# Kernel tuning notes

Hardware: AMD Instinct MI355X
Metric: run time of the kernel (lower is better)

## Reference

```python
import jax, jax.numpy as jnp
import numpy as np

N_NODES = 100000
N_EDGES = 1600000


def setup_inputs() -> dict:
    key = jax.random.key(0)
    k1, k2, k3, k4 = jax.random.split(key, 4)
    x = jax.random.normal(k1, (N_NODES, 128), dtype=jnp.float32)
    edge_idx = jax.random.randint(k2, (2, N_EDGES), 0, N_NODES, dtype=jnp.int64)
    W1 = jax.random.normal(k3, (128, 64), dtype=jnp.float32) * (1.0 / np.sqrt(128))
    b1 = jnp.zeros((64,), dtype=jnp.float32)
    W2 = jax.random.normal(k4, (64, 40), dtype=jnp.float32) * (1.0 / np.sqrt(64))
    b2 = jnp.zeros((40,), dtype=jnp.float32)
    return {"x": x, "edge_idx": edge_idx, "W1": W1, "b1": b1, "W2": W2, "b2": b2}


def _gcn_conv(x, src, dst, norm, W, b, n_nodes):
    # x @ W -> gather by src, scale by symmetric norm, scatter-add to dst, + bias
    h = x @ W                               # [N, d_out]
    msg = h[src] * norm[:, None]            # [E+N, d_out]
    out = jax.ops.segment_sum(msg, dst, num_segments=n_nodes)
    return out + b


def _norm_and_loops(edge_idx, n_nodes):
    # PyG GCNConv default: add self-loops, norm = deg^-1/2[src] * deg^-1/2[dst]
    loops = jnp.arange(n_nodes, dtype=edge_idx.dtype)
    src = jnp.concatenate([edge_idx[0], loops])
    dst = jnp.concatenate([edge_idx[1], loops])
    deg = jnp.zeros((n_nodes,), jnp.float32).at[dst].add(1.0)
    dinv = jnp.where(deg > 0, jax.lax.rsqrt(deg), 0.0)
    norm = dinv[src] * dinv[dst]
    return src, dst, norm


def reference(x, edge_idx, W1, b1, W2, b2):
    n_nodes = x.shape[0]
    src, dst, norm = _norm_and_loops(edge_idx, n_nodes)
    hidden = jax.nn.relu(_gcn_conv(x, src, dst, norm, W1, b1, n_nodes))
    # dropout is a no-op in eval mode (training=False)
    return _gcn_conv(hidden, src, dst, norm, W2, b2, n_nodes)
```

## Files before the change

kernel.cpp:

```cpp
#include <hip/hip_runtime.h>

#define D_IN  128
#define D_HID 64
#define D_OUT 40

__global__ __launch_bounds__(256) void k_deg(const int* __restrict__ dst,
                                             unsigned int* __restrict__ cnt,
                                             unsigned int* __restrict__ rank, int E) {
    int e = blockIdx.x * 256 + threadIdx.x;
    if (e < E) rank[e] = atomicAdd(&cnt[dst[e]], 1u);
}

__global__ __launch_bounds__(256) void k_dinv(const unsigned int* __restrict__ deg,
                                              float* __restrict__ dinv, int N) {
    int i = blockIdx.x * 256 + threadIdx.x;
    if (i < N) dinv[i] = rsqrtf((float)(deg[i] + 1u));
}

__global__ __launch_bounds__(256) void k_scan1(const unsigned int* __restrict__ deg,
                                               unsigned int* __restrict__ off,
                                               unsigned int* __restrict__ bsum, int N) {
    __shared__ unsigned int s[256];
    const int tid = threadIdx.x;
    const int i = blockIdx.x * 256 + tid;
    unsigned int v = (i < N) ? deg[i] : 0u;
    s[tid] = v;
    __syncthreads();
    for (int d = 1; d < 256; d <<= 1) {
        unsigned int t = (tid >= d) ? s[tid - d] : 0u;
        __syncthreads();
        s[tid] += t;
        __syncthreads();
    }
    if (i < N) off[i] = s[tid] - v;
    if (tid == 255) bsum[blockIdx.x] = s[tid];
}

__global__ __launch_bounds__(512) void k_scan2(unsigned int* __restrict__ bsum, int NB) {
    __shared__ unsigned int s[512];
    const int tid = threadIdx.x;
    unsigned int v = (tid < NB) ? bsum[tid] : 0u;
    s[tid] = v;
    __syncthreads();
    for (int d = 1; d < 512; d <<= 1) {
        unsigned int t = (tid >= d) ? s[tid - d] : 0u;
        __syncthreads();
        s[tid] += t;
        __syncthreads();
    }
    if (tid < NB) bsum[tid] = s[tid] - v;
}

__global__ __launch_bounds__(256) void k_scan3(unsigned int* __restrict__ off,
                                               const unsigned int* __restrict__ bsum,
                                               int N, int E) {
    int i = blockIdx.x * 256 + threadIdx.x;
    if (i < N) off[i] += bsum[blockIdx.x];
    if (i == 0) off[N] = (unsigned int)E;
}

__global__ __launch_bounds__(256) void k_fill(const int* __restrict__ src,
                                              const int* __restrict__ dst,
                                              const unsigned int* __restrict__ off,
                                              const unsigned int* __restrict__ rank,
                                              int* __restrict__ csr_src, int E) {
    int e = blockIdx.x * 256 + threadIdx.x;
    if (e >= E) return;
    csr_src[off[dst[e]] + rank[e]] = src[e];
}

__global__ __launch_bounds__(256) void k_gemm1(const float* __restrict__ x,
                                               const float* __restrict__ W1,
                                               const float* __restrict__ dinv,
                                               float* __restrict__ h1s, int N) {
    __shared__ float w[D_IN * D_HID];
    __shared__ float xs[16][D_IN + 4];
    const int tid = threadIdx.x;
    const float4* W4 = (const float4*)W1;
    float4* w4 = (float4*)w;
    for (int i = tid; i < D_IN * D_HID / 4; i += 256) w4[i] = W4[i];
    const int row0 = blockIdx.x * 16;
    const float4* X4 = (const float4*)(x + (size_t)row0 * D_IN);
    for (int i = tid; i < 16 * D_IN / 4; i += 256) {
        float4 v = X4[i];
        int r = i >> 5;
        int k = (i & 31) * 4;
        *(float4*)&xs[r][k] = v;
    }
    __syncthreads();
    const int r  = tid >> 4;
    const int c4 = (tid & 15) * 4;
    float a0 = 0, a1 = 0, a2 = 0, a3 = 0;
#pragma unroll 8
    for (int k = 0; k < D_IN; ++k) {
        float  xv = xs[r][k];
        float4 wv = *(const float4*)&w[k * D_HID + c4];
        a0 = fmaf(xv, wv.x, a0);
        a1 = fmaf(xv, wv.y, a1);
        a2 = fmaf(xv, wv.z, a2);
        a3 = fmaf(xv, wv.w, a3);
    }
    const int row = row0 + r;
    if (row < N) {
        float dv = dinv[row];
        float4 o = {a0 * dv, a1 * dv, a2 * dv, a3 * dv};
        *(float4*)&h1s[(size_t)row * D_HID + c4] = o;
    }
}

__global__ __launch_bounds__(320) void k_gemm2(const float* __restrict__ hid,
                                               const float* __restrict__ W2,
                                               const float* __restrict__ dinv,
                                               float* __restrict__ h2s, int N) {
    __shared__ float w[D_HID * D_OUT];
    __shared__ float xs[16][D_HID + 4];
    const int tid = threadIdx.x;
    const float2* W22 = (const float2*)W2;
    float2* w2 = (float2*)w;
    for (int i = tid; i < D_HID * D_OUT / 2; i += 320) w2[i] = W22[i];
    const int row0 = blockIdx.x * 16;
    const float4* X4 = (const float4*)(hid + (size_t)row0 * D_HID);
    for (int i = tid; i < 16 * D_HID / 4; i += 320) {
        float4 v = X4[i];
        int r = i >> 4;
        int k = (i & 15) * 4;
        *(float4*)&xs[r][k] = v;
    }
    __syncthreads();
    const int r  = tid / 20;
    const int c2 = (tid % 20) * 2;
    float a0 = 0, a1 = 0;
#pragma unroll 8
    for (int k = 0; k < D_HID; ++k) {
        float  xv = xs[r][k];
        float2 wv = *(const float2*)&w[k * D_OUT + c2];
        a0 = fmaf(xv, wv.x, a0);
        a1 = fmaf(xv, wv.y, a1);
    }
    const int row = row0 + r;
    if (row < N) {
        float dv = dinv[row];
        float2 o = {a0 * dv, a1 * dv};
        *(float2*)&h2s[(size_t)row * D_OUT + c2] = o;
    }
}

__global__ __launch_bounds__(256) void k_gather1(const unsigned int* __restrict__ off,
                                                 const int* __restrict__ csr_src,
                                                 const float* __restrict__ h1s,
                                                 const float* __restrict__ dinv,
                                                 const float* __restrict__ b1,
                                                 float* __restrict__ hidden, int N) {
    const int wid  = (blockIdx.x * 256 + threadIdx.x) >> 6;
    const int lane = threadIdx.x & 63;
    if (wid >= N) return;
    const int start = (int)off[wid];
    const int end   = (int)off[wid + 1];
    float acc = h1s[(size_t)wid * D_HID + lane];
    for (int base = start; base < end; base += 64) {
        const int nb = min(64, end - base);
        int sv = (base + lane < end) ? csr_src[base + lane] : 0;
        int j = 0;
        for (; j + 3 < nb; j += 4) {
            int s0 = __shfl(sv, j),     s1 = __shfl(sv, j + 1);
            int s2 = __shfl(sv, j + 2), s3 = __shfl(sv, j + 3);
            float v0 = h1s[(size_t)s0 * D_HID + lane];
            float v1 = h1s[(size_t)s1 * D_HID + lane];
            float v2 = h1s[(size_t)s2 * D_HID + lane];
            float v3 = h1s[(size_t)s3 * D_HID + lane];
            acc += (v0 + v1) + (v2 + v3);
        }
        for (; j < nb; ++j) {
            int s = __shfl(sv, j);
            acc += h1s[(size_t)s * D_HID + lane];
        }
    }
    float v = dinv[wid] * acc + b1[lane];
    hidden[(size_t)wid * D_HID + lane] = v > 0.0f ? v : 0.0f;
}

__global__ __launch_bounds__(256) void k_gather2(const unsigned int* __restrict__ off,
                                                 const int* __restrict__ csr_src,
                                                 const float* __restrict__ h2s,
                                                 const float* __restrict__ dinv,
                                                 const float* __restrict__ b2,
                                                 float* __restrict__ out, int N) {
    const int wid  = (blockIdx.x * 256 + threadIdx.x) >> 6;
    const int lane = threadIdx.x & 63;
    if (wid >= N) return;
    const int start = (int)off[wid];
    const int end   = (int)off[wid + 1];
    const bool act = lane < D_OUT;
    float acc = act ? h2s[(size_t)wid * D_OUT + lane] : 0.0f;
    for (int base = start; base < end; base += 64) {
        const int nb = min(64, end - base);
        int sv = (base + lane < end) ? csr_src[base + lane] : 0;
        int j = 0;
        for (; j + 3 < nb; j += 4) {
            int s0 = __shfl(sv, j),     s1 = __shfl(sv, j + 1);
            int s2 = __shfl(sv, j + 2), s3 = __shfl(sv, j + 3);
            if (act) {
                float v0 = h2s[(size_t)s0 * D_OUT + lane];
                float v1 = h2s[(size_t)s1 * D_OUT + lane];
                float v2 = h2s[(size_t)s2 * D_OUT + lane];
                float v3 = h2s[(size_t)s3 * D_OUT + lane];
                acc += (v0 + v1) + (v2 + v3);
            }
        }
        for (; j < nb; ++j) {
            int s = __shfl(sv, j);
            if (act) acc += h2s[(size_t)s * D_OUT + lane];
        }
    }
    if (act) out[(size_t)wid * D_OUT + lane] = dinv[wid] * acc + b2[lane];
}

extern "C" void kernel_launch(void* const* d_in, const int* in_sizes, int n_in,
                              void* d_out, int out_size, void* d_ws, size_t ws_size,
                              hipStream_t stream) {
    const float* x  = (const float*)d_in[0];
    const int*  eix = (const int*)d_in[1];
    const float* W1 = (const float*)d_in[2];
    const float* b1 = (const float*)d_in[3];
    const float* W2 = (const float*)d_in[4];
    const float* b2 = (const float*)d_in[5];
    float* out = (float*)d_out;

    const int N = in_sizes[0] / D_IN;
    const int E = in_sizes[1] / 2;
    const int* src = eix;
    const int* dst = eix + E;
    const int NB = (N + 255) / 256;

    char* ws = (char*)d_ws;
    size_t off_b = 0;
    auto alloc = [&](size_t bytes) {
        void* p = ws + off_b;
        off_b = (off_b + bytes + 255) & ~(size_t)255;
        return p;
    };
    unsigned int* deg     = (unsigned int*)alloc((size_t)N * 4);
    float*        dinv    = (float*)alloc((size_t)N * 4);
    unsigned int* offsets = (unsigned int*)alloc((size_t)(N + 1) * 4);
    unsigned int* bsums   = (unsigned int*)alloc(512 * 4);
    int*          csr_src = (int*)alloc((size_t)E * 4);
    float*        h1s     = (float*)alloc((size_t)N * D_HID * 4);
    float*        hidden  = (float*)alloc((size_t)N * D_HID * 4);
    float*        h2s     = h1s;
    unsigned int* rank    = (unsigned int*)hidden;

    hipMemsetAsync(deg, 0, (size_t)N * 4, stream);

    k_deg  <<<(E + 255) / 256, 256, 0, stream>>>(dst, deg, rank, E);
    k_dinv <<<NB, 256, 0, stream>>>(deg, dinv, N);
    k_scan1<<<NB, 256, 0, stream>>>(deg, offsets, bsums, N);
    k_scan2<<<1, 512, 0, stream>>>(bsums, NB);
    k_scan3<<<NB, 256, 0, stream>>>(offsets, bsums, N, E);
    k_fill <<<(E + 255) / 256, 256, 0, stream>>>(src, dst, offsets, rank, csr_src, E);

    k_gemm1  <<<(N + 15) / 16, 256, 0, stream>>>(x, W1, dinv, h1s, N);
    k_gather1<<<(N + 3) / 4, 256, 0, stream>>>(offsets, csr_src, h1s, dinv, b1, hidden, N);

    k_gemm2  <<<(N + 15) / 16, 320, 0, stream>>>(hidden, W2, dinv, h2s, N);
    k_gather2<<<(N + 3) / 4, 256, 0, stream>>>(offsets, csr_src, h2s, dinv, b2, out, N);
}
```

Baseline: 383.4 us.

## Store pre-aggregation features in bf16 and gather two nodes per wavefront

```diff
diff --git a/kernel.cpp b/kernel.cpp
--- a/kernel.cpp
+++ b/kernel.cpp
@@ -3,6 +3,18 @@
 #define D_IN  128
 #define D_HID 64
 #define D_OUT 40
+
+static __device__ __forceinline__ unsigned short f2bf(float f) {
+    unsigned int u = __float_as_uint(f);
+    unsigned int r = (u + 0x7fffu + ((u >> 16) & 1u)) >> 16;
+    return (unsigned short)r;
+}
+static __device__ __forceinline__ float bflo(unsigned int u) {
+    return __uint_as_float(u << 16);
+}
+static __device__ __forceinline__ float bfhi(unsigned int u) {
+    return __uint_as_float(u & 0xffff0000u);
+}
 
 __global__ __launch_bounds__(256) void k_deg(const int* __restrict__ dst,
                                              unsigned int* __restrict__ cnt,
@@ -11,19 +23,15 @@
     if (e < E) rank[e] = atomicAdd(&cnt[dst[e]], 1u);
 }
 
-__global__ __launch_bounds__(256) void k_dinv(const unsigned int* __restrict__ deg,
-                                              float* __restrict__ dinv, int N) {
-    int i = blockIdx.x * 256 + threadIdx.x;
-    if (i < N) dinv[i] = rsqrtf((float)(deg[i] + 1u));
-}
-
 __global__ __launch_bounds__(256) void k_scan1(const unsigned int* __restrict__ deg,
                                                unsigned int* __restrict__ off,
-                                               unsigned int* __restrict__ bsum, int N) {
+                                               unsigned int* __restrict__ bsum,
+                                               float* __restrict__ dinv, int N) {
     __shared__ unsigned int s[256];
     const int tid = threadIdx.x;
     const int i = blockIdx.x * 256 + tid;
     unsigned int v = (i < N) ? deg[i] : 0u;
+    if (i < N) dinv[i] = rsqrtf((float)(v + 1u));
     s[tid] = v;
     __syncthreads();
     for (int d = 1; d < 256; d <<= 1) {
@@ -72,7 +80,7 @@
 __global__ __launch_bounds__(256) void k_gemm1(const float* __restrict__ x,
                                                const float* __restrict__ W1,
                                                const float* __restrict__ dinv,
-                                               float* __restrict__ h1s, int N) {
+                                               unsigned short* __restrict__ h1s, int N) {
     __shared__ float w[D_IN * D_HID];
     __shared__ float xs[16][D_IN + 4];
     const int tid = threadIdx.x;
@@ -103,15 +111,17 @@
     const int row = row0 + r;
     if (row < N) {
         float dv = dinv[row];
-        float4 o = {a0 * dv, a1 * dv, a2 * dv, a3 * dv};
-        *(float4*)&h1s[(size_t)row * D_HID + c4] = o;
+        uint2 o;
+        o.x = (unsigned)f2bf(a0 * dv) | ((unsigned)f2bf(a1 * dv) << 16);
+        o.y = (unsigned)f2bf(a2 * dv) | ((unsigned)f2bf(a3 * dv) << 16);
+        *(uint2*)&h1s[(size_t)row * D_HID + c4] = o;
     }
 }
 
 __global__ __launch_bounds__(320) void k_gemm2(const float* __restrict__ hid,
                                                const float* __restrict__ W2,
                                                const float* __restrict__ dinv,
-                                               float* __restrict__ h2s, int N) {
+                                               unsigned short* __restrict__ h2s, int N) {
     __shared__ float w[D_HID * D_OUT];
     __shared__ float xs[16][D_HID + 4];
     const int tid = threadIdx.x;
@@ -140,79 +150,109 @@
     const int row = row0 + r;
     if (row < N) {
         float dv = dinv[row];
-        float2 o = {a0 * dv, a1 * dv};
-        *(float2*)&h2s[(size_t)row * D_OUT + c2] = o;
+        unsigned int o = (unsigned)f2bf(a0 * dv) | ((unsigned)f2bf(a1 * dv) << 16);
+        *(unsigned int*)&h2s[(size_t)row * D_OUT + c2] = o;
     }
 }
 
 __global__ __launch_bounds__(256) void k_gather1(const unsigned int* __restrict__ off,
                                                  const int* __restrict__ csr_src,
-                                                 const float* __restrict__ h1s,
+                                                 const unsigned int* __restrict__ h1s,
                                                  const float* __restrict__ dinv,
                                                  const float* __restrict__ b1,
                                                  float* __restrict__ hidden, int N) {
-    const int wid  = (blockIdx.x * 256 + threadIdx.x) >> 6;
+    const int gtid = blockIdx.x * 256 + threadIdx.x;
+    const int wid2 = gtid >> 6;
     const int lane = threadIdx.x & 63;
-    if (wid >= N) return;
-    const int start = (int)off[wid];
-    const int end   = (int)off[wid + 1];
-    float acc = h1s[(size_t)wid * D_HID + lane];
-    for (int base = start; base < end; base += 64) {
-        const int nb = min(64, end - base);
-        int sv = (base + lane < end) ? csr_src[base + lane] : 0;
+    const int half = lane >> 5;
+    const int hl   = lane & 31;
+    const int node = wid2 * 2 + half;
+    if (node >= N) return;
+    const int start = (int)off[node];
+    const int end   = (int)off[node + 1];
+    unsigned int u = h1s[(size_t)node * 32 + hl];
+    float a0 = bflo(u), a1 = bfhi(u);
+    for (int base = start; base < end; base += 32) {
+        const int nb = min(32, end - base);
+        int sv = (base + hl < end) ? csr_src[base + hl] : 0;
         int j = 0;
         for (; j + 3 < nb; j += 4) {
-            int s0 = __shfl(sv, j),     s1 = __shfl(sv, j + 1);
-            int s2 = __shfl(sv, j + 2), s3 = __shfl(sv, j + 3);
-            float v0 = h1s[(size_t)s0 * D_HID + lane];
-            float v1 = h1s[(size_t)s1 * D_HID + lane];
-            float v2 = h1s[(size_t)s2 * D_HID + lane];
-            float v3 = h1s[(size_t)s3 * D_HID + lane];
-            acc += (v0 + v1) + (v2 + v3);
+            int s0 = __shfl(sv, j, 32),     s1 = __shfl(sv, j + 1, 32);
+            int s2 = __shfl(sv, j + 2, 32), s3 = __shfl(sv, j + 3, 32);
+            unsigned int u0 = h1s[(size_t)s0 * 32 + hl];
+            unsigned int u1 = h1s[(size_t)s1 * 32 + hl];
+            unsigned int u2 = h1s[(size_t)s2 * 32 + hl];
+            unsigned int u3 = h1s[(size_t)s3 * 32 + hl];
+            a0 += (bflo(u0) + bflo(u1)) + (bflo(u2) + bflo(u3));
+            a1 += (bfhi(u0) + bfhi(u1)) + (bfhi(u2) + bfhi(u3));
         }
         for (; j < nb; ++j) {
-            int s = __shfl(sv, j);
-            acc += h1s[(size_t)s * D_HID + lane];
+            int s = __shfl(sv, j, 32);
+            unsigned int uu = h1s[(size_t)s * 32 + hl];
+            a0 += bflo(uu);
+            a1 += bfhi(uu);
         }
     }
-    float v = dinv[wid] * acc + b1[lane];
-    hidden[(size_t)wid * D_HID + lane] = v > 0.0f ? v : 0.0f;
+    const float dv = dinv[node];
+    const float2 bb = *(const float2*)&b1[hl * 2];
+    float v0 = dv * a0 + bb.x;
+    float v1 = dv * a1 + bb.y;
+    float2 o = {v0 > 0.0f ? v0 : 0.0f, v1 > 0.0f ? v1 : 0.0f};
+    *(float2*)&hidden[(size_t)node * D_HID + hl * 2] = o;
 }
 
 __global__ __launch_bounds__(256) void k_gather2(const unsigned int* __restrict__ off,
                                                  const int* __restrict__ csr_src,
-                                                 const float* __restrict__ h2s,
+                                                 const unsigned int* __restrict__ h2s,
                                                  const float* __restrict__ dinv,
                                                  const float* __restrict__ b2,
                                                  float* __restrict__ out, int N) {
-    const int wid  = (blockIdx.x * 256 + threadIdx.x) >> 6;
+    const int gtid = blockIdx.x * 256 + threadIdx.x;
+    const int wid2 = gtid >> 6;
     const int lane = threadIdx.x & 63;
-    if (wid >= N) return;
-    const int start = (int)off[wid];
-    const int end   = (int)off[wid + 1];
-    const bool act = lane < D_OUT;
-    float acc = act ? h2s[(size_t)wid * D_OUT + lane] : 0.0f;
-    for (int base = start; base < end; base += 64) {
-        const int nb = min(64, end - base);
-        int sv = (base + lane < end) ? csr_src[base + lane] : 0;
+    const int half = lane >> 5;
+    const int hl   = lane & 31;
+    const int node = wid2 * 2 + half;
+    if (node >= N) return;
+    const int start = (int)off[node];
+    const int end   = (int)off[node + 1];
+    const bool act = hl < 20;
+    float a0 = 0.0f, a1 = 0.0f;
+    if (act) {
+        unsigned int u = h2s[(size_t)node * 20 + hl];
+        a0 = bflo(u); a1 = bfhi(u);
+    }
+    for (int base = start; base < end; base += 32) {
+        const int nb = min(32, end - base);
+        int sv = (base + hl < end) ? csr_src[base + hl] : 0;
         int j = 0;
         for (; j + 3 < nb; j += 4) {
-            int s0 = __shfl(sv, j),     s1 = __shfl(sv, j + 1);
-            int s2 = __shfl(sv, j + 2), s3 = __shfl(sv, j + 3);
+            int s0 = __shfl(sv, j, 32),     s1 = __shfl(sv, j + 1, 32);
+            int s2 = __shfl(sv, j + 2, 32), s3 = __shfl(sv, j + 3, 32);
             if (act) {
-                float v0 = h2s[(size_t)s0 * D_OUT + lane];
-                float v1 = h2s[(size_t)s1 * D_OUT + lane];
-                float v2 = h2s[(size_t)s2 * D_OUT + lane];
-                float v3 = h2s[(size_t)s3 * D_OUT + lane];
-                acc += (v0 + v1) + (v2 + v3);
+                unsigned int u0 = h2s[(size_t)s0 * 20 + hl];
+                unsigned int u1 = h2s[(size_t)s1 * 20 + hl];
+                unsigned int u2 = h2s[(size_t)s2 * 20 + hl];
+                unsigned int u3 = h2s[(size_t)s3 * 20 + hl];
+                a0 += (bflo(u0) + bflo(u1)) + (bflo(u2) + bflo(u3));
+                a1 += (bfhi(u0) + bfhi(u1)) + (bfhi(u2) + bfhi(u3));
             }
         }
         for (; j < nb; ++j) {
-            int s = __shfl(sv, j);
-            if (act) acc += h2s[(size_t)s * D_OUT + lane];
+            int s = __shfl(sv, j, 32);
+            if (act) {
+                unsigned int uu = h2s[(size_t)s * 20 + hl];
+                a0 += bflo(uu);
+                a1 += bfhi(uu);
+            }
         }
     }
-    if (act) out[(size_t)wid * D_OUT + lane] = dinv[wid] * acc + b2[lane];
+    if (act) {
+        const float dv = dinv[node];
+        const float2 bb = *(const float2*)&b2[hl * 2];
+        float2 o = {dv * a0 + bb.x, dv * a1 + bb.y};
+        *(float2*)&out[(size_t)node * D_OUT + hl * 2] = o;
+    }
 }
 
 extern "C" void kernel_launch(void* const* d_in, const int* in_sizes, int n_in,
@@ -239,28 +279,30 @@
         off_b = (off_b + bytes + 255) & ~(size_t)255;
         return p;
     };
-    unsigned int* deg     = (unsigned int*)alloc((size_t)N * 4);
-    float*        dinv    = (float*)alloc((size_t)N * 4);
-    unsigned int* offsets = (unsigned int*)alloc((size_t)(N + 1) * 4);
-    unsigned int* bsums   = (unsigned int*)alloc(512 * 4);
-    int*          csr_src = (int*)alloc((size_t)E * 4);
-    float*        h1s     = (float*)alloc((size_t)N * D_HID * 4);
-    float*        hidden  = (float*)alloc((size_t)N * D_HID * 4);
-    float*        h2s     = h1s;
-    unsigned int* rank    = (unsigned int*)hidden;
+    unsigned int*   deg     = (unsigned int*)alloc((size_t)N * 4);
+    float*          dinv    = (float*)alloc((size_t)N * 4);
+    unsigned int*   offsets = (unsigned int*)alloc((size_t)(N + 1) * 4);
+    unsigned int*   bsums   = (unsigned int*)alloc(512 * 4);
+    int*            csr_src = (int*)alloc((size_t)E * 4);
+    unsigned short* h1s     = (unsigned short*)alloc((size_t)N * D_HID * 2);
+    float*          hidden  = (float*)alloc((size_t)N * D_HID * 4);
+    unsigned short* h2s     = h1s;
+    unsigned int*   rank    = (unsigned int*)hidden;
 
     hipMemsetAsync(deg, 0, (size_t)N * 4, stream);
 
     k_deg  <<<(E + 255) / 256, 256, 0, stream>>>(dst, deg, rank, E);
-    k_dinv <<<NB, 256, 0, stream>>>(deg, dinv, N);
-    k_scan1<<<NB, 256, 0, stream>>>(deg, offsets, bsums, N);
+    k_scan1<<<NB, 256, 0, stream>>>(deg, offsets, bsums, dinv, N);
     k_scan2<<<1, 512, 0, stream>>>(bsums, NB);
     k_scan3<<<NB, 256, 0, stream>>>(offsets, bsums, N, E);
     k_fill <<<(E + 255) / 256, 256, 0, stream>>>(src, dst, offsets, rank, csr_src, E);
 
+    const int gwaves = (N + 1) / 2;
+    const int gblocks = (gwaves + 3) / 4;
+
     k_gemm1  <<<(N + 15) / 16, 256, 0, stream>>>(x, W1, dinv, h1s, N);
-    k_gather1<<<(N + 3) / 4, 256, 0, stream>>>(offsets, csr_src, h1s, dinv, b1, hidden, N);
+    k_gather1<<<gblocks, 256, 0, stream>>>(offsets, csr_src, (const unsigned int*)h1s, dinv, b1, hidden, N);
 
     k_gemm2  <<<(N + 15) / 16, 320, 0, stream>>>(hidden, W2, dinv, h2s, N);
-    k_gather2<<<(N + 3) / 4, 256, 0, stream>>>(offsets, csr_src, h2s, dinv, b2, out, N);
-}
+    k_gather2<<<gblocks, 256, 0, stream>>>(offsets, csr_src, (const unsigned int*)h2s, dinv, b2, out, N);
+}
```

New measurement: 340.2 us. 1.13x faster.
